# Kernel tuning notes

Measured on AMD Instinct MI355X. Metric: run time of the kernel, lower is better.

## Reference

```python
import jax, jax.numpy as jnp
import numpy as np

B, C, H, W = 4, 256, 64, 64
CH = C // 2  # inner channels


def setup_inputs() -> dict:
    key = jax.random.key(0)
    ks = jax.random.split(key, 9)
    s = 1.0 / np.sqrt(C)
    so = 1.0 / np.sqrt(CH)
    return {
        "x": jax.random.normal(ks[0], (B, C, H, W), dtype=jnp.float32),
        "teta_w": jax.random.uniform(ks[1], (CH, C), jnp.float32, -s, s),
        "teta_b": jax.random.uniform(ks[2], (CH,), jnp.float32, -s, s),
        "fi_w": jax.random.uniform(ks[3], (CH, C), jnp.float32, -s, s),
        "fi_b": jax.random.uniform(ks[4], (CH,), jnp.float32, -s, s),
        "gi_w": jax.random.uniform(ks[5], (CH, C), jnp.float32, -s, s),
        "gi_b": jax.random.uniform(ks[6], (CH,), jnp.float32, -s, s),
        "out_w": jax.random.uniform(ks[7], (C, CH), jnp.float32, -so, so),
        "out_b": jax.random.uniform(ks[8], (C,), jnp.float32, -so, so),
    }


def _conv1x1(x, w, b):
    # x: (B, Cin, H, W), w: (Cout, Cin) -> (B, Cout, H, W)
    return jnp.einsum('bchw,oc->bohw', x, w) + b[None, :, None, None]


def reference(x, teta_w, teta_b, fi_w, fi_b, gi_w, gi_b, out_w, out_b):
    b, c, h, w = x.shape
    n = h * w
    ch = teta_w.shape[0]
    # NOTE: original uses .view (reshape), NOT transpose, to get (B, N, Ch)
    x1 = _conv1x1(x, teta_w, teta_b).reshape(b, ch, n).reshape(b, n, ch)
    x2 = _conv1x1(x, fi_w, fi_b).reshape(b, ch, n)            # (B, Ch, N)
    x3 = _conv1x1(x, gi_w, gi_b).reshape(b, ch, n).reshape(b, n, ch)
    # softmax over dim=1 (rows), as in the original
    attn = jax.nn.softmax(jnp.matmul(x1, x2), axis=1)          # (B, N, N)
    y = jnp.matmul(attn, x3)                                   # (B, N, Ch)
    y = jnp.swapaxes(y, 1, 2).reshape(b, ch, h, w)
    return x + _conv1x1(y, out_w, out_b)
```

## Files before the change

kernel.cpp:

```cpp
#include <hip/hip_runtime.h>
#include <hip/hip_bf16.h>

#define BB 4
#define CC 256
#define CHH 128
#define NN 4096
#define KSHIFT 12.0f

typedef __attribute__((ext_vector_type(8))) short bf16x8;
typedef __attribute__((ext_vector_type(4))) float f32x4;

__device__ __forceinline__ float to_f(float v) { return v; }
__device__ __forceinline__ float to_f(__hip_bfloat16 v) { return __bfloat162float(v); }
__device__ __forceinline__ void st_f(float* p, float v) { *p = v; }
__device__ __forceinline__ void st_f(__hip_bfloat16* p, float v) { *p = __float2bfloat16(v); }
__device__ __forceinline__ unsigned short f2bf(float f) {
    __hip_bfloat16 h = __float2bfloat16(f);
    unsigned short u;
    __builtin_memcpy(&u, &h, 2);
    return u;
}
__device__ __forceinline__ bf16x8 ldb8(const unsigned short* p) { return *(const bf16x8*)p; }

__device__ __forceinline__ void gload_lds16(const unsigned short* g, unsigned short* l) {
    __builtin_amdgcn_global_load_lds(
        (const __attribute__((address_space(1))) unsigned int*)g,
        (__attribute__((address_space(3))) unsigned int*)l, 16, 0, 0);
}

__global__ void detect_kernel(const void* __restrict__ tb, int* __restrict__ flag) {
    if (threadIdx.x == 0) {
        const __hip_bfloat16* p = (const __hip_bfloat16*)tb;
        int big = 0, zeros = 0;
        for (int i = 0; i < 128; ++i) {
            float v = __bfloat162float(p[i]);
            if (!(fabsf(v) <= 0.5f)) big = 1;
            if ((i & 1) == 0 && v == 0.0f) zeros++;
        }
        *flag = (big || zeros >= 32) ? 1 : 0;
    }
}

template <typename T>
__device__ __forceinline__ void prep_body(const T* tw, const T* fw, const T* gw, const T* ow,
                                          const T* tb2, const T* fb, const T* gb, const T* ob,
                                          unsigned short* Wb, unsigned short* OWb,
                                          float* Bf, float* OBf) {
    int idx = blockIdx.x * 256 + threadIdx.x;
    if (idx < 98304) {
        int cv = idx >> 15, rem = idx & 32767;
        const T* src = cv == 0 ? tw : (cv == 1 ? fw : gw);
        Wb[idx] = f2bf(to_f(src[rem]));
    } else if (idx < 131072) {
        OWb[idx - 98304] = f2bf(to_f(ow[idx - 98304]));
    } else if (idx < 131456) {
        int r = idx - 131072;
        int cv = r >> 7, j = r & 127;
        const T* src = cv == 0 ? tb2 : (cv == 1 ? fb : gb);
        Bf[r] = to_f(src[j]);
    } else if (idx < 131712) {
        OBf[idx - 131456] = to_f(ob[idx - 131456]);
    }
}

__global__ void prep_kernel(const void* tw, const void* fw, const void* gw, const void* ow,
                            const void* tb2, const void* fb, const void* gb, const void* ob,
                            const int* __restrict__ flag,
                            unsigned short* Wb, unsigned short* OWb, float* Bf, float* OBf) {
    if (*flag)
        prep_body<float>((const float*)tw, (const float*)fw, (const float*)gw, (const float*)ow,
                         (const float*)tb2, (const float*)fb, (const float*)gb, (const float*)ob,
                         Wb, OWb, Bf, OBf);
    else
        prep_body<__hip_bfloat16>((const __hip_bfloat16*)tw, (const __hip_bfloat16*)fw,
                                  (const __hip_bfloat16*)gw, (const __hip_bfloat16*)ow,
                                  (const __hip_bfloat16*)tb2, (const __hip_bfloat16*)fb,
                                  (const __hip_bfloat16*)gb, (const __hip_bfloat16*)ob,
                                  Wb, OWb, Bf, OBf);
}

template <typename T>
__device__ __forceinline__ void xtrans_body(const T* __restrict__ x, unsigned short* __restrict__ xt) {
    int b = blockIdx.z;
    const T* in = x + (size_t)b * CC * NN;
    unsigned short* out = xt + (size_t)b * NN * CC;
    int p0 = blockIdx.x * 64, c0 = blockIdx.y * 64;
    __shared__ unsigned short t[64][68];
    int flat = threadIdx.x;
#pragma unroll
    for (int tt = 0; tt < 16; ++tt) {
        int id = flat + tt * 256;
        int rr = id >> 6, cc = id & 63;
        t[cc][rr] = f2bf(to_f(in[(size_t)(c0 + rr) * NN + p0 + cc]));
    }
    __syncthreads();
#pragma unroll
    for (int tt = 0; tt < 16; ++tt) {
        int id = flat + tt * 256;
        int pp = id >> 6, jj = id & 63;
        out[(size_t)(p0 + pp) * CC + c0 + jj] = t[pp][jj];
    }
}

__launch_bounds__(256)
__global__ void xtrans_kernel(const void* x, const int* __restrict__ flag,
                              unsigned short* __restrict__ xt) {
    if (*flag) xtrans_body<float>((const float*)x, xt);
    else       xtrans_body<__hip_bfloat16>((const __hip_bfloat16*)x, xt);
}

__launch_bounds__(256)
__global__ void conv3_mfma_kernel(const unsigned short* __restrict__ xt,
                                  const unsigned short* __restrict__ Wb,
                                  const float* __restrict__ Bf,
                                  unsigned short* __restrict__ T1b,
                                  unsigned short* __restrict__ T2t,
                                  unsigned short* __restrict__ T3b) {
    int b = blockIdx.y;
    int p0 = blockIdx.x * 16;
    int flat = threadIdx.x;
    int w = flat >> 6, lane = flat & 63, m = lane & 15, quad = lane >> 4;
    const unsigned short* xrow = xt + ((size_t)b * NN + p0 + m) * CC;
    bf16x8 xf[8];
#pragma unroll
    for (int kc = 0; kc < 8; ++kc)
        xf[kc] = ldb8(&xrow[kc * 32 + quad * 8]);
    unsigned short* t1  = T1b + (size_t)b * CHH * NN;
    unsigned short* t2t = T2t + (size_t)b * CHH * NN;
    unsigned short* t3  = T3b + (size_t)b * CHH * NN;
#pragma unroll
    for (int q = 0; q < 6; ++q) {
        int t = w * 6 + q;
        int cv = t >> 3, ot = t & 7;
        int o0 = ot * 16;
        const unsigned short* wrow = Wb + ((size_t)cv * CHH + o0 + m) * CC;
        f32x4 acc = {0.f, 0.f, 0.f, 0.f};
#pragma unroll
        for (int kc = 0; kc < 8; ++kc) {
            bf16x8 wf = ldb8(&wrow[kc * 32 + quad * 8]);
            acc = __builtin_amdgcn_mfma_f32_16x16x32_bf16(wf, xf[kc], acc, 0, 0, 0);
        }
        unsigned short hv[4];
#pragma unroll
        for (int r = 0; r < 4; ++r)
            hv[r] = f2bf(acc[r] + Bf[cv * CHH + o0 + quad * 4 + r]);
        if (cv == 1) {
            unsigned int lo = (unsigned int)hv[0] | ((unsigned int)hv[1] << 16);
            unsigned int hi = (unsigned int)hv[2] | ((unsigned int)hv[3] << 16);
            int src = (lane & 3) * 16 + (lane >> 2);
            unsigned int tlo = (unsigned int)__shfl((int)lo, src, 64);
            unsigned int thi = (unsigned int)__shfl((int)hi, src, 64);
            unsigned int* dst = (unsigned int*)&t2t[(size_t)(p0 + (lane >> 2)) * CHH +
                                                    o0 + (lane & 3) * 4];
            dst[0] = tlo;
            dst[1] = thi;
        } else {
            unsigned short* outp = (cv == 0) ? t1 : t3;
#pragma unroll
            for (int r = 0; r < 4; ++r)
                outp[(size_t)(o0 + quad * 4 + r) * NN + p0 + m] = hv[r];
        }
    }
}

__launch_bounds__(256)
__global__ void transpose_kernel(const unsigned short* __restrict__ in,
                                 unsigned short* __restrict__ out, int R, int C) {
    int bz = blockIdx.z;
    in  += (size_t)bz * R * C;
    out += (size_t)bz * R * C;
    int c0 = blockIdx.x * 64, r0 = blockIdx.y * 64;
    __shared__ unsigned short t[64][68];
    int flat = threadIdx.x;
#pragma unroll
    for (int tt = 0; tt < 16; ++tt) {
        int id = flat + tt * 256;
        int r = id >> 6, c = id & 63;
        t[c][r] = in[(size_t)(r0 + r) * C + c0 + c];
    }
    __syncthreads();
#pragma unroll
    for (int tt = 0; tt < 16; ++tt) {
        int id = flat + tt * 256;
        int c = id >> 6, r = id & 63;
        out[(size_t)(c0 + c) * R + r0 + r] = t[c][r];
    }
}

__launch_bounds__(256)
__global__ void stats_mfma_kernel(const unsigned short* __restrict__ T1b,
                                  const unsigned short* __restrict__ T2t,
                                  float* __restrict__ Lpart) {
    int blk = blockIdx.x;
    int b = (blk & 7) >> 1;
    int rest = (blk >> 3) * 2 + (blk & 1);
    int strip = rest >> 3, iq = rest & 7;
    int ibase = iq * 512;
    int flat = threadIdx.x;
    int w = flat >> 6, lane = flat & 63, m = lane & 15, quad = lane >> 4;
    const unsigned short* A  = T1b + (size_t)b * CHH * NN;
    const unsigned short* Bt = T2t + (size_t)b * CHH * NN;
    __shared__ unsigned short th[2][64 * 128];

    int u0w = strip * 128 + w * 32;
    bf16x8 bfr[2][4];
#pragma unroll
    for (int g = 0; g < 2; ++g)
#pragma unroll
        for (int kc = 0; kc < 4; ++kc)
            bfr[g][kc] = ldb8(&Bt[(size_t)(u0w + g * 16 + m) * CHH + kc * 32 + quad * 8]);

#define STAGE_TH(dst, ii)                                                          \
    _Pragma("unroll")                                                              \
    for (int i_ = 0; i_ < 4; ++i_) {                                               \
        int sl = i_ * 256 + flat;                                                  \
        int r_ = sl >> 4, ch_ = sl & 15;                                           \
        int c_ = ch_ ^ (r_ & 7);                                                   \
        gload_lds16(&A[(size_t)((ii) + r_) * CHH + c_ * 8], &th[dst][sl * 8]);     \
    }

    float csum[2] = {0.f, 0.f};
    STAGE_TH(0, ibase);
    __syncthreads();
    int cur = 0;
    for (int t = 0; t < 8; ++t) {
        if (t < 7) { STAGE_TH(cur ^ 1, ibase + (t + 1) * 64); }
        const unsigned short* thc = th[cur];
#pragma unroll
        for (int s = 0; s < 4; ++s) {
            int irow = s * 16 + m;
            bf16x8 af[4];
#pragma unroll
            for (int kc = 0; kc < 4; ++kc) {
                int ch = (kc * 4 + quad) ^ (irow & 7);
                af[kc] = *(const bf16x8*)&thc[irow * 128 + ch * 8];
            }
#pragma unroll
            for (int g = 0; g < 2; ++g) {
                f32x4 acc = {0.f, 0.f, 0.f, 0.f};
#pragma unroll
                for (int kc = 0; kc < 4; ++kc)
                    acc = __builtin_amdgcn_mfma_f32_16x16x32_bf16(af[kc], bfr[g][kc], acc, 0, 0, 0);
#pragma unroll
                for (int r = 0; r < 4; ++r)
                    csum[g] += __expf(acc[r] - KSHIFT);
            }
        }
        if (t < 7) {
            __syncthreads();
            cur ^= 1;
        }
    }
#undef STAGE_TH
#pragma unroll
    for (int g = 0; g < 2; ++g) {
        csum[g] += __shfl_xor(csum[g], 16, 64);
        csum[g] += __shfl_xor(csum[g], 32, 64);
        if (lane < 16)
            Lpart[((size_t)iq * BB + b) * NN + u0w + g * 16 + m] = csum[g];
    }
}

__launch_bounds__(512, 2)
__global__ void attn_mfma_kernel(const unsigned short* __restrict__ T1b,
                                 const unsigned short* __restrict__ T2t,
                                 const unsigned short* __restrict__ X3t,
                                 const float* __restrict__ Lpart,
                                 unsigned short* __restrict__ Yp0,
                                 unsigned short* __restrict__ Yp1,
                                 unsigned short* __restrict__ Yp2,
                                 unsigned short* __restrict__ Yp3) {
    int blk = blockIdx.x;
    int b = (blk & 7) >> 1;
    int rest = (blk >> 3) * 2 + (blk & 1);
    int it = rest >> 2, uc = rest & 3;
    int i0 = it * 128;
    unsigned short* Yp = uc == 0 ? Yp0 : (uc == 1 ? Yp1 : (uc == 2 ? Yp2 : Yp3));
    int flat = threadIdx.x;
    int w = flat >> 6, lane = flat & 63, m = lane & 15, quad = lane >> 4;
    int ig = w & 3, h = w >> 2;
    const unsigned short* A  = T1b + (size_t)b * CHH * NN;
    const unsigned short* Bt = T2t + (size_t)b * CHH * NN;
    const unsigned short* X3 = X3t + (size_t)b * CHH * NN;

    __shared__ __align__(16) unsigned char smem[69632];
    unsigned short* bt0 = (unsigned short*)smem;
    unsigned short* x3s = (unsigned short*)(smem + 32768);
    unsigned short* pTg = (unsigned short*)(smem + 49152) + ig * 2048;
    float* llh = (float*)(smem + 65536);

    int ubeg = uc * 1024;
#pragma unroll
    for (int k = 0; k < 2; ++k) {
        int idx = k * 512 + flat;
        int u = ubeg + idx;
        float s = 0.f;
#pragma unroll
        for (int c = 0; c < 8; ++c)
            s += Lpart[((size_t)c * BB + b) * NN + u];
        llh[idx] = logf(s) + KSHIFT;
    }

    int iw = i0 + ig * 32;
    int j0 = h * 64;
    bf16x8 ath[2][4];
#pragma unroll
    for (int g = 0; g < 2; ++g)
#pragma unroll
        for (int kc = 0; kc < 4; ++kc)
            ath[g][kc] = ldb8(&A[(size_t)(iw + g * 16 + m) * CHH + kc * 32 + quad * 8]);
    f32x4 yacc[2][4];
#pragma unroll
    for (int g = 0; g < 2; ++g)
#pragma unroll
        for (int js = 0; js < 4; ++js) yacc[g][js] = (f32x4){0.f, 0.f, 0.f, 0.f};

#define STAGE_BT(dst, uu)                                                          \
    _Pragma("unroll")                                                              \
    for (int i_ = 0; i_ < 2; ++i_) {                                    \
        int sl = i_ * 512 + flat;                                                  \
        int u_ = sl >> 4, ch_ = sl & 15;                                           \
        int c_ = ch_ ^ (u_ & 7);                                                   \
        gload_lds16(&Bt[(size_t)((uu) + u_) * CHH + c_ * 8],                       \
                    bt0 + (dst) * 8192 + sl * 8);                                  \
    }
#define STAGE_X3(uu)                                                               \
    _Pragma("unroll")                                                              \
    for (int i_ = 0; i_ < 2; ++i_) {                                    \
        int sl = i_ * 512 + flat;                                                  \
        int j_ = sl >> 3, ch_ = sl & 7;                                            \
        int c_ = ch_ ^ (j_ & 7);                                                   \
        gload_lds16(&X3[(size_t)j_ * NN + (uu) + c_ * 8], x3s + sl * 8);           \
    }

    STAGE_BT(0, ubeg);
    STAGE_X3(ubeg);
    __syncthreads();
    int cur = 0;
    for (int t = 0; t < 16; ++t) {
        int u0 = ubeg + t * 64;
        if (t < 15) { STAGE_BT(cur ^ 1, u0 + 64); }
        const unsigned short* btc = bt0 + cur * 8192;
#pragma unroll
        for (int su = 0; su < 2; ++su) {
            int ul = h * 32 + su * 16 + m;
            f32x4 a0 = {0.f, 0.f, 0.f, 0.f}, a1 = {0.f, 0.f, 0.f, 0.f};
#pragma unroll
            for (int kc = 0; kc < 4; ++kc) {
                int ch = (kc * 4 + quad) ^ (ul & 7);
                bf16x8 bf = *(const bf16x8*)&btc[ul * 128 + ch * 8];
                a0 = __builtin_amdgcn_mfma_f32_16x16x32_bf16(ath[0][kc], bf, a0, 0, 0, 0);
                a1 = __builtin_amdgcn_mfma_f32_16x16x32_bf16(ath[1][kc], bf, a1, 0, 0, 0);
            }
            float ll = llh[u0 - ubeg + ul];
#pragma unroll
            for (int r = 0; r < 4; ++r) {
                int r0 = quad * 4 + r;
                pTg[r0 * 64 + ((ul >> 3) ^ (r0 & 7)) * 8 + (ul & 7)] =
                    f2bf(__expf(a0[r] - ll));
                pTg[(16 + r0) * 64 + ((ul >> 3) ^ (r0 & 7)) * 8 + (ul & 7)] =
                    f2bf(__expf(a1[r] - ll));
            }
        }
        __syncthreads();
#pragma unroll
        for (int ku = 0; ku < 2; ++ku) {
            bf16x8 pa0 = *(const bf16x8*)&pTg[m * 64 + ((ku * 4 + quad) ^ (m & 7)) * 8];
            bf16x8 pa1 = *(const bf16x8*)&pTg[(16 + m) * 64 + ((ku * 4 + quad) ^ (m & 7)) * 8];
#pragma unroll
            for (int js = 0; js < 4; ++js) {
                int j = j0 + js * 16 + m;
                int ch = (ku * 4 + quad) ^ (j & 7);
                bf16x8 xb = *(const bf16x8*)&x3s[j * 64 + ch * 8];
                yacc[0][js] = __builtin_amdgcn_mfma_f32_16x16x32_bf16(pa0, xb, yacc[0][js], 0, 0, 0);
                yacc[1][js] = __builtin_amdgcn_mfma_f32_16x16x32_bf16(pa1, xb, yacc[1][js], 0, 0, 0);
            }
        }
        __syncthreads();
        if (t < 15) { STAGE_X3(u0 + 64); }
        cur ^= 1;
    }
#undef STAGE_BT
#undef STAGE_X3
#pragma unroll
    for (int g = 0; g < 2; ++g)
#pragma unroll
        for (int js = 0; js < 4; ++js)
#pragma unroll
            for (int r = 0; r < 4; ++r)
                Yp[((size_t)b * NN + iw + g * 16 + quad * 4 + r) * CHH +
                   j0 + js * 16 + m] = f2bf(yacc[g][js][r]);
}

template <typename T>
__device__ __forceinline__ void outconv_body(const T* __restrict__ x,
                                             const unsigned short* __restrict__ Yp0,
                                             const unsigned short* __restrict__ Yp1,
                                             const unsigned short* __restrict__ Yp2,
                                             const unsigned short* __restrict__ Yp3,
                                             const unsigned short* __restrict__ OWb,
                                             const float* __restrict__ OBf,
                                             T* __restrict__ out) {
    int b = blockIdx.y;
    int p0 = blockIdx.x * 16;
    int flat = threadIdx.x;
    int w = flat >> 6, lane = flat & 63, m = lane & 15, quad = lane >> 4;
    size_t yoff = ((size_t)b * NN + p0 + m) * CHH;
    const unsigned short* yrows[4] = {Yp0 + yoff, Yp1 + yoff, Yp2 + yoff, Yp3 + yoff};
    bf16x8 yf[4][4];
#pragma unroll
    for (int pz = 0; pz < 4; ++pz)
#pragma unroll
        for (int kc = 0; kc < 4; ++kc)
            yf[pz][kc] = ldb8(&yrows[pz][kc * 32 + quad * 8]);
#pragma unroll
    for (int q = 0; q < 4; ++q) {
        int o0 = (w * 4 + q) * 16;
        const unsigned short* wrow = OWb + (size_t)(o0 + m) * CHH;
        f32x4 acc = {0.f, 0.f, 0.f, 0.f};
#pragma unroll
        for (int kc = 0; kc < 4; ++kc) {
            bf16x8 aw = ldb8(&wrow[kc * 32 + quad * 8]);
#pragma unroll
            for (int pz = 0; pz < 4; ++pz)
                acc = __builtin_amdgcn_mfma_f32_16x16x32_bf16(aw, yf[pz][kc], acc, 0, 0, 0);
        }
#pragma unroll
        for (int r = 0; r < 4; ++r) {
            int co = o0 + quad * 4 + r;
            size_t oi = ((size_t)b * CC + co) * NN + p0 + m;
            st_f(&out[oi], acc[r] + OBf[co] + to_f(x[oi]));
        }
    }
}

__launch_bounds__(256)
__global__ void outconv_mfma_kernel(const void* x,
                                    const unsigned short* __restrict__ Yp0,
                                    const unsigned short* __restrict__ Yp1,
                                    const unsigned short* __restrict__ Yp2,
                                    const unsigned short* __restrict__ Yp3,
                                    const unsigned short* __restrict__ OWb,
                                    const float* __restrict__ OBf,
                                    const int* __restrict__ flag, void* out) {
    if (*flag)
        outconv_body<float>((const float*)x, Yp0, Yp1, Yp2, Yp3, OWb, OBf, (float*)out);
    else
        outconv_body<__hip_bfloat16>((const __hip_bfloat16*)x, Yp0, Yp1, Yp2, Yp3, OWb, OBf,
                                     (__hip_bfloat16*)out);
}

extern "C" void kernel_launch(void* const* d_in, const int* in_sizes, int n_in,
                              void* d_out, int out_size, void* d_ws, size_t ws_size,
                              hipStream_t stream) {
    const void* x  = d_in[0];
    const void* tw = d_in[1];
    const void* tb = d_in[2];
    const void* fw = d_in[3];
    const void* fb = d_in[4];
    const void* gw = d_in[5];
    const void* gb = d_in[6];
    const void* ow = d_in[7];
    const void* ob = d_in[8];

    const size_t TE = (size_t)BB * CHH * NN;
    unsigned short* T1b = (unsigned short*)d_ws;
    unsigned short* T2t = T1b + TE;
    unsigned short* X3t = T2t + TE;
    unsigned short* T3b = X3t + TE;
    unsigned short* xt  = T3b + TE;
    unsigned short* Yp0 = xt;
    unsigned short* Yp1 = xt + TE;
    unsigned short* Yp2 = T3b;
    unsigned short* Yp3 = xt + 2 * TE;
    unsigned short* Wb  = Yp3 + TE;
    unsigned short* OWb = Wb + 98304;
    float* Bf    = (float*)(OWb + 32768);
    float* OBf   = Bf + 384;
    float* Lpart = OBf + 256;
    int*   Flag  = (int*)(Lpart + 131072);

    detect_kernel<<<1, 64, 0, stream>>>(tb, Flag);
    prep_kernel<<<dim3(515), 256, 0, stream>>>(tw, fw, gw, ow, tb, fb, gb, ob,
                                               Flag, Wb, OWb, Bf, OBf);
    xtrans_kernel<<<dim3(NN / 64, CC / 64, BB), 256, 0, stream>>>(x, Flag, xt);
    conv3_mfma_kernel<<<dim3(NN / 16, BB), 256, 0, stream>>>(xt, Wb, Bf, T1b, T2t, T3b);
    transpose_kernel<<<dim3(CHH / 64, NN / 64, BB), 256, 0, stream>>>(T3b, X3t, NN, CHH);
    stats_mfma_kernel<<<dim3(1024), 256, 0, stream>>>(T1b, T2t, Lpart);
    attn_mfma_kernel<<<dim3(512), 512, 0, stream>>>(T1b, T2t, X3t, Lpart, Yp0, Yp1, Yp2, Yp3);
    outconv_mfma_kernel<<<dim3(NN / 16, BB), 256, 0, stream>>>(x, Yp0, Yp1, Yp2, Yp3,
                                                               OWb, OBf, Flag, d_out);
}
```

Measured before the change: 208.2 us.

## Retile attention waves to 2x4 (i by j) and parallelize bias detection

The attention kernel's wave layout changes from 4 row groups × 2 column halves to 2 row groups of 64 rows × 4 output-column quarters. Each wave now computes a 16-column slice of the score tile for 64 rows and reads P from a 64x64 tile shared by four waves. The MFMA count per wave is unchanged, but LDS traffic for the T2 and X3 tiles drops while P reads rise, at the cost of holding twice as many A fragments in registers. That raises register pressure under the 512-thread, 2-block launch bound and risks spills. Separately, the dtype-detection kernel is rewritten to read its 128 values across threads with wave ballots instead of a single-thread loop.

```diff
diff --git a/kernel.cpp b/kernel.cpp
--- a/kernel.cpp
+++ b/kernel.cpp
@@ -29,16 +29,19 @@
 }
 
 __global__ void detect_kernel(const void* __restrict__ tb, int* __restrict__ flag) {
-    if (threadIdx.x == 0) {
-        const __hip_bfloat16* p = (const __hip_bfloat16*)tb;
-        int big = 0, zeros = 0;
-        for (int i = 0; i < 128; ++i) {
-            float v = __bfloat162float(p[i]);
-            if (!(fabsf(v) <= 0.5f)) big = 1;
-            if ((i & 1) == 0 && v == 0.0f) zeros++;
-        }
-        *flag = (big || zeros >= 32) ? 1 : 0;
-    }
+    const __hip_bfloat16* p = (const __hip_bfloat16*)tb;
+    int i = threadIdx.x;
+    int big = 0, zero_even = 0;
+#pragma unroll
+    for (int k = 0; k < 2; ++k) {
+        int idx = i * 2 + k;
+        float v = __bfloat162float(p[idx]);
+        if (!(fabsf(v) <= 0.5f)) big = 1;
+        if ((idx & 1) == 0 && v == 0.0f) zero_even = 1;
+    }
+    unsigned long long bigm = __ballot(big);
+    unsigned long long zm = __ballot(zero_even);
+    if (i == 0) *flag = (bigm != 0ULL || __popcll(zm) >= 32) ? 1 : 0;
 }
 
 template <typename T>
@@ -278,7 +281,7 @@
     unsigned short* Yp = uc == 0 ? Yp0 : (uc == 1 ? Yp1 : (uc == 2 ? Yp2 : Yp3));
     int flat = threadIdx.x;
     int w = flat >> 6, lane = flat & 63, m = lane & 15, quad = lane >> 4;
-    int ig = w & 3, h = w >> 2;
+    int jq = w & 3, ig = w >> 2;
     const unsigned short* A  = T1b + (size_t)b * CHH * NN;
     const unsigned short* Bt = T2t + (size_t)b * CHH * NN;
     const unsigned short* X3 = X3t + (size_t)b * CHH * NN;
@@ -286,7 +289,7 @@
     __shared__ __align__(16) unsigned char smem[69632];
     unsigned short* bt0 = (unsigned short*)smem;
     unsigned short* x3s = (unsigned short*)(smem + 32768);
-    unsigned short* pTg = (unsigned short*)(smem + 49152) + ig * 2048;
+    unsigned short* pTg = (unsigned short*)(smem + 49152) + ig * 4096;
     float* llh = (float*)(smem + 65536);
 
     int ubeg = uc * 1024;
@@ -301,19 +304,19 @@
         llh[idx] = logf(s) + KSHIFT;
     }
 
-    int iw = i0 + ig * 32;
-    int j0 = h * 64;
-    bf16x8 ath[2][4];
-#pragma unroll
-    for (int g = 0; g < 2; ++g)
+    int iw = i0 + ig * 64;
+    int j0 = jq * 32;
+    bf16x8 ath[4][4];
+#pragma unroll
+    for (int g = 0; g < 4; ++g)
 #pragma unroll
         for (int kc = 0; kc < 4; ++kc)
             ath[g][kc] = ldb8(&A[(size_t)(iw + g * 16 + m) * CHH + kc * 32 + quad * 8]);
-    f32x4 yacc[2][4];
-#pragma unroll
-    for (int g = 0; g < 2; ++g)
-#pragma unroll
-        for (int js = 0; js < 4; ++js) yacc[g][js] = (f32x4){0.f, 0.f, 0.f, 0.f};
+    f32x4 yacc[4][2];
+#pragma unroll
+    for (int g = 0; g < 4; ++g)
+#pragma unroll
+        for (int js = 0; js < 2; ++js) yacc[g][js] = (f32x4){0.f, 0.f, 0.f, 0.f};
 
 #define STAGE_BT(dst, uu)                                                          \
     _Pragma("unroll")                                                              \
@@ -341,39 +344,45 @@
         int u0 = ubeg + t * 64;
         if (t < 15) { STAGE_BT(cur ^ 1, u0 + 64); }
         const unsigned short* btc = bt0 + cur * 8192;
-#pragma unroll
-        for (int su = 0; su < 2; ++su) {
-            int ul = h * 32 + su * 16 + m;
-            f32x4 a0 = {0.f, 0.f, 0.f, 0.f}, a1 = {0.f, 0.f, 0.f, 0.f};
+        {
+            int ul = jq * 16 + m;
+            f32x4 sa[4];
+#pragma unroll
+            for (int g = 0; g < 4; ++g) sa[g] = (f32x4){0.f, 0.f, 0.f, 0.f};
 #pragma unroll
             for (int kc = 0; kc < 4; ++kc) {
                 int ch = (kc * 4 + quad) ^ (ul & 7);
                 bf16x8 bf = *(const bf16x8*)&btc[ul * 128 + ch * 8];
-                a0 = __builtin_amdgcn_mfma_f32_16x16x32_bf16(ath[0][kc], bf, a0, 0, 0, 0);
-                a1 = __builtin_amdgcn_mfma_f32_16x16x32_bf16(ath[1][kc], bf, a1, 0, 0, 0);
+#pragma unroll
+                for (int g = 0; g < 4; ++g)
+                    sa[g] = __builtin_amdgcn_mfma_f32_16x16x32_bf16(ath[g][kc], bf, sa[g], 0, 0, 0);
             }
-            float ll = llh[u0 - ubeg + ul];
+            float ll = llh[t * 64 + ul];
 #pragma unroll
             for (int r = 0; r < 4; ++r) {
-                int r0 = quad * 4 + r;
-                pTg[r0 * 64 + ((ul >> 3) ^ (r0 & 7)) * 8 + (ul & 7)] =
-                    f2bf(__expf(a0[r] - ll));
-                pTg[(16 + r0) * 64 + ((ul >> 3) ^ (r0 & 7)) * 8 + (ul & 7)] =
-                    f2bf(__expf(a1[r] - ll));
+                int rr = quad * 4 + r;
+                int sw = ((ul >> 3) ^ (rr & 7)) * 8 + (ul & 7);
+#pragma unroll
+                for (int g = 0; g < 4; ++g)
+                    pTg[(g * 16 + rr) * 64 + sw] = f2bf(__expf(sa[g][r] - ll));
             }
         }
         __syncthreads();
 #pragma unroll
         for (int ku = 0; ku < 2; ++ku) {
-            bf16x8 pa0 = *(const bf16x8*)&pTg[m * 64 + ((ku * 4 + quad) ^ (m & 7)) * 8];
-            bf16x8 pa1 = *(const bf16x8*)&pTg[(16 + m) * 64 + ((ku * 4 + quad) ^ (m & 7)) * 8];
-#pragma unroll
-            for (int js = 0; js < 4; ++js) {
+            bf16x8 pa[4];
+#pragma unroll
+            for (int g = 0; g < 4; ++g)
+                pa[g] = *(const bf16x8*)&pTg[(g * 16 + m) * 64 +
+                                             ((ku * 4 + quad) ^ (m & 7)) * 8];
+#pragma unroll
+            for (int js = 0; js < 2; ++js) {
                 int j = j0 + js * 16 + m;
                 int ch = (ku * 4 + quad) ^ (j & 7);
                 bf16x8 xb = *(const bf16x8*)&x3s[j * 64 + ch * 8];
-                yacc[0][js] = __builtin_amdgcn_mfma_f32_16x16x32_bf16(pa0, xb, yacc[0][js], 0, 0, 0);
-                yacc[1][js] = __builtin_amdgcn_mfma_f32_16x16x32_bf16(pa1, xb, yacc[1][js], 0, 0, 0);
+#pragma unroll
+                for (int g = 0; g < 4; ++g)
+                    yacc[g][js] = __builtin_amdgcn_mfma_f32_16x16x32_bf16(pa[g], xb, yacc[g][js], 0, 0, 0);
             }
         }
         __syncthreads();
@@ -383,9 +392,9 @@
 #undef STAGE_BT
 #undef STAGE_X3
 #pragma unroll
-    for (int g = 0; g < 2; ++g)
-#pragma unroll
-        for (int js = 0; js < 4; ++js)
+    for (int g = 0; g < 4; ++g)
+#pragma unroll
+        for (int js = 0; js < 2; ++js)
 #pragma unroll
             for (int r = 0; r < 4; ++r)
                 Yp[((size_t)b * NN + iw + g * 16 + quad * 4 + r) * CHH +
```

Result: no change. 208.2 us (-0.0%).

## Merge detect, prep and xtrans kernels; fuse transpose into stats launch

Applied to the files above, without the earlier changes.

Removes the separate single-thread dtype-detect kernel: each block now detects the input dtype with a wave ballot into shared memory. Weight prep and the x transpose are merged into one launch, and the T3 transpose is folded into the stats kernel as extra blocks sharing one LDS arena. This cuts the launch count from eight to five and removes the serial detect kernel plus the launch gaps between dependent small kernels. Every block now repeats the small detect read, and the stats blocks' LDS footprint and occupancy stay the same.

```diff
diff --git a/kernel.cpp b/kernel.cpp
--- a/kernel.cpp
+++ b/kernel.cpp
@@ -28,17 +28,24 @@
         (__attribute__((address_space(3))) unsigned int*)l, 16, 0, 0);
 }
 
-__global__ void detect_kernel(const void* __restrict__ tb, int* __restrict__ flag) {
-    if (threadIdx.x == 0) {
+__device__ __forceinline__ int detect_flag_block(const void* tb, int* sflag) {
+    int tid = threadIdx.x;
+    if (tid < 64) {
         const __hip_bfloat16* p = (const __hip_bfloat16*)tb;
-        int big = 0, zeros = 0;
-        for (int i = 0; i < 128; ++i) {
-            float v = __bfloat162float(p[i]);
+        int big = 0, zero_even = 0;
+#pragma unroll
+        for (int k = 0; k < 2; ++k) {
+            int idx = tid * 2 + k;
+            float v = __bfloat162float(p[idx]);
             if (!(fabsf(v) <= 0.5f)) big = 1;
-            if ((i & 1) == 0 && v == 0.0f) zeros++;
-        }
-        *flag = (big || zeros >= 32) ? 1 : 0;
-    }
+            if ((idx & 1) == 0 && v == 0.0f) zero_even = 1;
+        }
+        unsigned long long bigm = __ballot(big);
+        unsigned long long zm = __ballot(zero_even);
+        if (tid == 0) *sflag = (bigm != 0ULL || __popcll(zm) >= 32) ? 1 : 0;
+    }
+    __syncthreads();
+    return *sflag;
 }
 
 template <typename T>
@@ -63,50 +70,55 @@
     }
 }
 
-__global__ void prep_kernel(const void* tw, const void* fw, const void* gw, const void* ow,
-                            const void* tb2, const void* fb, const void* gb, const void* ob,
-                            const int* __restrict__ flag,
-                            unsigned short* Wb, unsigned short* OWb, float* Bf, float* OBf) {
-    if (*flag)
-        prep_body<float>((const float*)tw, (const float*)fw, (const float*)gw, (const float*)ow,
-                         (const float*)tb2, (const float*)fb, (const float*)gb, (const float*)ob,
-                         Wb, OWb, Bf, OBf);
-    else
-        prep_body<__hip_bfloat16>((const __hip_bfloat16*)tw, (const __hip_bfloat16*)fw,
-                                  (const __hip_bfloat16*)gw, (const __hip_bfloat16*)ow,
-                                  (const __hip_bfloat16*)tb2, (const __hip_bfloat16*)fb,
-                                  (const __hip_bfloat16*)gb, (const __hip_bfloat16*)ob,
-                                  Wb, OWb, Bf, OBf);
-}
-
 template <typename T>
-__device__ __forceinline__ void xtrans_body(const T* __restrict__ x, unsigned short* __restrict__ xt) {
-    int b = blockIdx.z;
+__device__ __forceinline__ void xtrans_body(const T* __restrict__ x, unsigned short* __restrict__ xt,
+                                            int id, unsigned short (*t)[68]) {
+    int b = id >> 8;
     const T* in = x + (size_t)b * CC * NN;
     unsigned short* out = xt + (size_t)b * NN * CC;
-    int p0 = blockIdx.x * 64, c0 = blockIdx.y * 64;
+    int p0 = (id & 63) * 64, c0 = ((id >> 6) & 3) * 64;
+    int flat = threadIdx.x;
+#pragma unroll
+    for (int tt = 0; tt < 16; ++tt) {
+        int idd = flat + tt * 256;
+        int rr = idd >> 6, cc = idd & 63;
+        t[cc][rr] = f2bf(to_f(in[(size_t)(c0 + rr) * NN + p0 + cc]));
+    }
+    __syncthreads();
+#pragma unroll
+    for (int tt = 0; tt < 16; ++tt) {
+        int idd = flat + tt * 256;
+        int pp = idd >> 6, jj = idd & 63;
+        out[(size_t)(p0 + pp) * CC + c0 + jj] = t[pp][jj];
+    }
+}
+
+__launch_bounds__(256)
+__global__ void prep_xtrans_kernel(const void* x,
+                                   const void* tw, const void* fw, const void* gw, const void* ow,
+                                   const void* tb2, const void* fb, const void* gb, const void* ob,
+                                   unsigned short* Wb, unsigned short* OWb,
+                                   float* Bf, float* OBf,
+                                   unsigned short* __restrict__ xt) {
+    __shared__ int sflag;
     __shared__ unsigned short t[64][68];
-    int flat = threadIdx.x;
-#pragma unroll
-    for (int tt = 0; tt < 16; ++tt) {
-        int id = flat + tt * 256;
-        int rr = id >> 6, cc = id & 63;
-        t[cc][rr] = f2bf(to_f(in[(size_t)(c0 + rr) * NN + p0 + cc]));
-    }
-    __syncthreads();
-#pragma unroll
-    for (int tt = 0; tt < 16; ++tt) {
-        int id = flat + tt * 256;
-        int pp = id >> 6, jj = id & 63;
-        out[(size_t)(p0 + pp) * CC + c0 + jj] = t[pp][jj];
-    }
-}
-
-__launch_bounds__(256)
-__global__ void xtrans_kernel(const void* x, const int* __restrict__ flag,
-                              unsigned short* __restrict__ xt) {
-    if (*flag) xtrans_body<float>((const float*)x, xt);
-    else       xtrans_body<__hip_bfloat16>((const __hip_bfloat16*)x, xt);
+    int flag = detect_flag_block(tb2, &sflag);
+    if (blockIdx.x < 515) {
+        if (flag)
+            prep_body<float>((const float*)tw, (const float*)fw, (const float*)gw, (const float*)ow,
+                             (const float*)tb2, (const float*)fb, (const float*)gb, (const float*)ob,
+                             Wb, OWb, Bf, OBf);
+        else
+            prep_body<__hip_bfloat16>((const __hip_bfloat16*)tw, (const __hip_bfloat16*)fw,
+                                      (const __hip_bfloat16*)gw, (const __hip_bfloat16*)ow,
+                                      (const __hip_bfloat16*)tb2, (const __hip_bfloat16*)fb,
+                                      (const __hip_bfloat16*)gb, (const __hip_bfloat16*)ob,
+                                      Wb, OWb, Bf, OBf);
+    } else {
+        int id = blockIdx.x - 515;
+        if (flag) xtrans_body<float>((const float*)x, xt, id, t);
+        else      xtrans_body<__hip_bfloat16>((const __hip_bfloat16*)x, xt, id, t);
+    }
 }
 
 __launch_bounds__(256)
@@ -164,43 +176,45 @@
 }
 
 __launch_bounds__(256)
-__global__ void transpose_kernel(const unsigned short* __restrict__ in,
-                                 unsigned short* __restrict__ out, int R, int C) {
-    int bz = blockIdx.z;
-    in  += (size_t)bz * R * C;
-    out += (size_t)bz * R * C;
-    int c0 = blockIdx.x * 64, r0 = blockIdx.y * 64;
-    __shared__ unsigned short t[64][68];
+__global__ void trans_stats_kernel(const unsigned short* __restrict__ T1b,
+                                   const unsigned short* __restrict__ T2t,
+                                   const unsigned short* __restrict__ T3b,
+                                   unsigned short* __restrict__ X3t,
+                                   float* __restrict__ Lpart) {
+    __shared__ unsigned short arena[2 * 64 * 128];
     int flat = threadIdx.x;
-#pragma unroll
-    for (int tt = 0; tt < 16; ++tt) {
-        int id = flat + tt * 256;
-        int r = id >> 6, c = id & 63;
-        t[c][r] = in[(size_t)(r0 + r) * C + c0 + c];
-    }
-    __syncthreads();
-#pragma unroll
-    for (int tt = 0; tt < 16; ++tt) {
-        int id = flat + tt * 256;
-        int c = id >> 6, r = id & 63;
-        out[(size_t)(c0 + c) * R + r0 + r] = t[c][r];
-    }
-}
-
-__launch_bounds__(256)
-__global__ void stats_mfma_kernel(const unsigned short* __restrict__ T1b,
-                                  const unsigned short* __restrict__ T2t,
-                                  float* __restrict__ Lpart) {
+    if (blockIdx.x >= 1024) {
+        int id = blockIdx.x - 1024;
+        int bz = id >> 7;
+        int by = (id >> 1) & 63;
+        int bx = id & 1;
+        const unsigned short* in = T3b + (size_t)bz * NN * CHH;
+        unsigned short* out = X3t + (size_t)bz * NN * CHH;
+        int c0 = bx * 64, r0 = by * 64;
+        unsigned short (*t)[68] = (unsigned short (*)[68])arena;
+#pragma unroll
+        for (int tt = 0; tt < 16; ++tt) {
+            int id2 = flat + tt * 256;
+            int r = id2 >> 6, c = id2 & 63;
+            t[c][r] = in[(size_t)(r0 + r) * CHH + c0 + c];
+        }
+        __syncthreads();
+#pragma unroll
+        for (int tt = 0; tt < 16; ++tt) {
+            int id2 = flat + tt * 256;
+            int c = id2 >> 6, r = id2 & 63;
+            out[(size_t)(c0 + c) * NN + r0 + r] = t[c][r];
+        }
+        return;
+    }
     int blk = blockIdx.x;
     int b = (blk & 7) >> 1;
     int rest = (blk >> 3) * 2 + (blk & 1);
     int strip = rest >> 3, iq = rest & 7;
     int ibase = iq * 512;
-    int flat = threadIdx.x;
     int w = flat >> 6, lane = flat & 63, m = lane & 15, quad = lane >> 4;
     const unsigned short* A  = T1b + (size_t)b * CHH * NN;
     const unsigned short* Bt = T2t + (size_t)b * CHH * NN;
-    __shared__ unsigned short th[2][64 * 128];
 
     int u0w = strip * 128 + w * 32;
     bf16x8 bfr[2][4];
@@ -216,7 +230,8 @@
         int sl = i_ * 256 + flat;                                                  \
         int r_ = sl >> 4, ch_ = sl & 15;                                           \
         int c_ = ch_ ^ (r_ & 7);                                                   \
-        gload_lds16(&A[(size_t)((ii) + r_) * CHH + c_ * 8], &th[dst][sl * 8]);     \
+        gload_lds16(&A[(size_t)((ii) + r_) * CHH + c_ * 8],                        \
+                    arena + (dst) * 8192 + sl * 8);                                \
     }
 
     float csum[2] = {0.f, 0.f};
@@ -225,7 +240,7 @@
     int cur = 0;
     for (int t = 0; t < 8; ++t) {
         if (t < 7) { STAGE_TH(cur ^ 1, ibase + (t + 1) * 64); }
-        const unsigned short* thc = th[cur];
+        const unsigned short* thc = arena + cur * 8192;
 #pragma unroll
         for (int s = 0; s < 4; ++s) {
             int irow = s * 16 + m;
@@ -435,15 +450,17 @@
 }
 
 __launch_bounds__(256)
-__global__ void outconv_mfma_kernel(const void* x,
+__global__ void outconv_mfma_kernel(const void* x, const void* tb2,
                                     const unsigned short* __restrict__ Yp0,
                                     const unsigned short* __restrict__ Yp1,
                                     const unsigned short* __restrict__ Yp2,
                                     const unsigned short* __restrict__ Yp3,
                                     const unsigned short* __restrict__ OWb,
                                     const float* __restrict__ OBf,
-                                    const int* __restrict__ flag, void* out) {
-    if (*flag)
+                                    void* out) {
+    __shared__ int sflag;
+    int flag = detect_flag_block(tb2, &sflag);
+    if (flag)
         outconv_body<float>((const float*)x, Yp0, Yp1, Yp2, Yp3, OWb, OBf, (float*)out);
     else
         outconv_body<__hip_bfloat16>((const __hip_bfloat16*)x, Yp0, Yp1, Yp2, Yp3, OWb, OBf,
@@ -478,16 +495,12 @@
     float* Bf    = (float*)(OWb + 32768);
     float* OBf   = Bf + 384;
     float* Lpart = OBf + 256;
-    int*   Flag  = (int*)(Lpart + 131072);
-
-    detect_kernel<<<1, 64, 0, stream>>>(tb, Flag);
-    prep_kernel<<<dim3(515), 256, 0, stream>>>(tw, fw, gw, ow, tb, fb, gb, ob,
-                                               Flag, Wb, OWb, Bf, OBf);
-    xtrans_kernel<<<dim3(NN / 64, CC / 64, BB), 256, 0, stream>>>(x, Flag, xt);
+
+    prep_xtrans_kernel<<<dim3(1539), 256, 0, stream>>>(x, tw, fw, gw, ow, tb, fb, gb, ob,
+                                                       Wb, OWb, Bf, OBf, xt);
     conv3_mfma_kernel<<<dim3(NN / 16, BB), 256, 0, stream>>>(xt, Wb, Bf, T1b, T2t, T3b);
-    transpose_kernel<<<dim3(CHH / 64, NN / 64, BB), 256, 0, stream>>>(T3b, X3t, NN, CHH);
-    stats_mfma_kernel<<<dim3(1024), 256, 0, stream>>>(T1b, T2t, Lpart);
+    trans_stats_kernel<<<dim3(1536), 256, 0, stream>>>(T1b, T2t, T3b, X3t, Lpart);
     attn_mfma_kernel<<<dim3(512), 512, 0, stream>>>(T1b, T2t, X3t, Lpart, Yp0, Yp1, Yp2, Yp3);
-    outconv_mfma_kernel<<<dim3(NN / 16, BB), 256, 0, stream>>>(x, Yp0, Yp1, Yp2, Yp3,
-                                                               OWb, OBf, Flag, d_out);
-}
+    outconv_mfma_kernel<<<dim3(NN / 16, BB), 256, 0, stream>>>(x, tb, Yp0, Yp1, Yp2, Yp3,
+                                                               OWb, OBf, d_out);
+}
```

New measurement: 196.2 us. 1.06x faster.
